# Kernel optimization log

Measured on AMD Instinct MI355X. Metric: run time of the kernel, lower is better.

## Reference

```python
import jax, jax.numpy as jnp
import numpy as np

B, D_IN, H1, H2, A = 8192, 512, 4096, 4096, 64
QMIN, QMAX = -128.0, 127.0  # int8 saturation range


def _int_vals(key, shape, spread):
    # integer-valued fixed-point tensor stored as float32
    return jnp.clip(jnp.round(jax.random.normal(key, shape) * spread), QMIN * spread, QMAX * spread).astype(jnp.float32)


def setup_inputs() -> dict:
    key = jax.random.key(0)
    ks = jax.random.split(key, 9)
    x = jnp.clip(jnp.round(jax.random.normal(ks[0], (B, D_IN)) * 32.0), QMIN, QMAX).astype(jnp.float32)
    w1 = jnp.clip(jnp.round(jax.random.normal(ks[1], (H1, D_IN)) * 16.0), QMIN, QMAX).astype(jnp.float32)
    b1 = _int_vals(ks[2], (H1,), 256.0)
    w2 = jnp.clip(jnp.round(jax.random.normal(ks[3], (H2, H1)) * 16.0), QMIN, QMAX).astype(jnp.float32)
    b2 = _int_vals(ks[4], (H2,), 256.0)
    w_mu = jnp.clip(jnp.round(jax.random.normal(ks[5], (A, H2)) * 16.0), QMIN, QMAX).astype(jnp.float32)
    b_mu = _int_vals(ks[6], (A,), 256.0)
    w_prob = jnp.clip(jnp.round(jax.random.normal(ks[7], (A, H2)) * 16.0), QMIN, QMAX).astype(jnp.float32)
    b_prob = _int_vals(ks[8], (A,), 256.0)
    M = jnp.full((1,), 2.0 ** -10, dtype=jnp.float32)  # per-layer requant multiplier
    s = jnp.full((1,), 0.05, dtype=jnp.float32)        # activation quantize scale
    return {
        "x": x, "w1": w1, "b1": b1, "w2": w2, "b2": b2,
        "w_mu": w_mu, "b_mu": b_mu, "w_prob": w_prob, "b_prob": b_prob,
        "M1": M, "M2": M, "M_mu": M, "M_prob": M,
        "s2": s, "s_mu": s, "s_prob": s,
    }


def _qlinear(x, w, b, M):
    # genesys fixed-point linear: int accumulate then requantize by multiplier M
    acc = jnp.matmul(x, w.T) + b  # integer-valued fp32 accumulator
    return jnp.round(M * acc)


def _quantize(src, scale, zero_point=0.0):
    return jnp.clip(jnp.round(src / scale) + zero_point, QMIN, QMAX)


def reference(x, w1, b1, w2, b2, w_mu, b_mu, w_prob, b_prob, M1, M2, M_mu, M_prob, s2, s_mu, s_prob):
    h = jax.nn.relu(_qlinear(x, w1, b1, M1))
    h = _quantize(h, s2)
    h = jax.nn.relu(_qlinear(h, w2, b2, M2))
    # NOTE: original forward_int feeds the un-quantized relu output into the
    # heads (x_mu/x_prob quantizations are dead code) and returns only prob.
    prob = _qlinear(h, w_prob, b_prob, M_prob)
    return prob
```

## Files before the change

kernel.cpp:

```cpp
#include <hip/hip_runtime.h>
#include <stdint.h>

#define NB   8192
#define DIN  512
#define NH1  4096
#define NH2  4096
#define NA   64

typedef int v4i __attribute__((ext_vector_type(4)));

__device__ __forceinline__ v4i mfma_i8(v4i a, v4i b, v4i c) {
    return __builtin_amdgcn_mfma_i32_16x16x64_i8(a, b, c, 0, 0, 0);
}

__device__ __forceinline__ void gload16(const void* g, const void* l) {
    __builtin_amdgcn_global_load_lds(
        (const __attribute__((address_space(1))) void*)(uintptr_t)g,
        (__attribute__((address_space(3))) void*)(uint32_t)(uintptr_t)l,
        16, 0, 0);
}

__global__ void cvt_i8(const float* __restrict__ in, signed char* __restrict__ out, int n4) {
    const int i = blockIdx.x * blockDim.x + threadIdx.x;
    if (i >= n4) return;
    const float4 v = ((const float4*)in)[i];
    char4 c;
    c.x = (signed char)__float2int_rn(v.x);
    c.y = (signed char)__float2int_rn(v.y);
    c.z = (signed char)__float2int_rn(v.z);
    c.w = (signed char)__float2int_rn(v.w);
    ((char4*)out)[i] = c;
}

__global__ void sum_wp(const float* __restrict__ wp, int* __restrict__ S) {
    __shared__ int red[256];
    const int a = blockIdx.x, t = threadIdx.x;
    int p = 0;
    for (int k = t; k < NH2; k += 256) p += __float2int_rn(wp[(size_t)a * NH2 + k]);
    red[t] = p; __syncthreads();
    for (int s = 128; s > 0; s >>= 1) { if (t < s) red[t] += red[t + s]; __syncthreads(); }
    if (t == 0) S[a] = red[0];
}

template <int EPI>
__global__ __launch_bounds__(512, 4)
void gemm_ra(const signed char* __restrict__ Ag,
             const signed char* __restrict__ Bg,
             int M, int N, int K,
             const float* __restrict__ bias,
             const float* __restrict__ Mscale,
             const float* __restrict__ qscale,
             signed char* __restrict__ out0,
             signed char* __restrict__ out1)
{
    __shared__ __align__(16) signed char lds[3][24576];

    const int tid  = threadIdx.x;
    const int lane = tid & 63;
    const int wid  = tid >> 6;
    const int wm   = wid >> 1, wn = wid & 1;

    const int nwg  = gridDim.x;
    const int bid  = blockIdx.x;
    const int swzb = (bid & 7) * (nwg >> 3) + (bid >> 3);
    const int nbx  = N >> 7;
    const int bx   = swzb % nbx;
    const int by   = swzb / nbx;
    const int bm0  = by << 8, bn0 = bx << 7;

    const int srow = tid >> 2;
    const int sc   = (((tid & 3) ^ ((tid >> 3) & 3)) << 4);
    const signed char* aS = Ag + (size_t)(bm0 + srow) * K + sc;
    const signed char* bS = Bg + (size_t)(bn0 + srow) * K + sc;
    const size_t rK = (size_t)128 * K;

#define STG(bp, t) do { \
    const int ko_ = (t) << 6; \
    gload16(aS + ko_,      &lds[bp][0]     + tid * 16); \
    gload16(aS + rK + ko_, &lds[bp][8192]  + tid * 16); \
    gload16(bS + ko_,      &lds[bp][16384] + tid * 16); } while (0)

    const int r    = lane & 15;
    const int pc   = (((lane >> 4) ^ ((r >> 1) & 3)) << 4);
    const int aoff = wm * 4096 + r * 64 + pc;
    const int boff = 16384 + wn * 4096 + r * 64 + pc;

    const int nt = K >> 6;

    STG(0, 0);
    STG(1, 1);
    asm volatile("s_waitcnt vmcnt(3)" ::: "memory");
    __builtin_amdgcn_s_barrier();

    v4i af[4], bf[4];
    {
        const signed char* L = &lds[0][0];
        #pragma unroll
        for (int m = 0; m < 4; ++m) af[m] = *(const v4i*)(L + aoff + m * 1024);
        #pragma unroll
        for (int n = 0; n < 4; ++n) bf[n] = *(const v4i*)(L + boff + n * 1024);
    }

    v4i acc[4][4] = {};
    int cur = 0;

    for (int t = 0; t < nt; ++t) {
        if (t + 2 < nt) {
            const int nb = (cur == 0) ? 2 : cur - 1;
            STG(nb, t + 2);
            asm volatile("s_waitcnt vmcnt(3)" ::: "memory");
        } else {
            asm volatile("s_waitcnt vmcnt(0)" ::: "memory");
        }
        __builtin_amdgcn_s_barrier();

        const int nxt = (cur == 2) ? 0 : cur + 1;
        const signed char* Ln = &lds[nxt][0];

        __builtin_amdgcn_s_setprio(1);
        #pragma unroll
        for (int m = 0; m < 4; ++m) {
            #pragma unroll
            for (int n = 0; n < 4; ++n)
                acc[m][n] = mfma_i8(af[m], bf[n], acc[m][n]);
            af[m] = *(const v4i*)(Ln + aoff + m * 1024);
        }
        __builtin_amdgcn_s_setprio(0);
        #pragma unroll
        for (int n = 0; n < 4; ++n) bf[n] = *(const v4i*)(Ln + boff + n * 1024);

        cur = nxt;
    }
#undef STG

    __syncthreads();
    signed char* img0 = (signed char*)&lds[0][0];
    signed char* img1 = img0 + 34816;
    const int rowb = wm * 64 + ((lane >> 4) << 2);
    const int colb = wn * 64 + (lane & 15);

#define FLUSH(dst, img) do { \
    _Pragma("unroll") \
    for (int p = 0; p < 8; ++p) { \
        const int idx = p * 512 + tid; \
        const int row = idx >> 4; \
        const int cb  = (idx & 15) * 8; \
        *(int2*)((dst) + (size_t)(bm0 + row) * N + bn0 + cb) = \
            *(const int2*)((img) + row * 136 + cb); \
    } } while (0)

    if constexpr (EPI == 1) {
        const float Mv = Mscale[0];
        const float sv = qscale[0];
        #pragma unroll
        for (int n = 0; n < 4; ++n) {
            const int col  = colb + n * 16;
            const int bint = __float2int_rn(bias[bn0 + col]);
            #pragma unroll
            for (int m = 0; m < 4; ++m) {
                #pragma unroll
                for (int j = 0; j < 4; ++j) {
                    const int row  = rowb + m * 16 + j;
                    const int accv = acc[m][n][j] + bint;
                    float h = rintf(Mv * (float)accv);
                    h = fmaxf(h, 0.0f);
                    float q = rintf(h / sv);
                    q = fminf(fmaxf(q, -128.0f), 127.0f);
                    img0[row * 136 + col] = (signed char)(int)q;
                }
            }
        }
        __syncthreads();
        FLUSH(out0, img0);
    } else {
        const float Mv = Mscale[0];
        #pragma unroll
        for (int n = 0; n < 4; ++n) {
            const int col  = colb + n * 16;
            const int bint = __float2int_rn(bias[bn0 + col]);
            #pragma unroll
            for (int m = 0; m < 4; ++m) {
                #pragma unroll
                for (int j = 0; j < 4; ++j) {
                    const int row  = rowb + m * 16 + j;
                    const int accv = acc[m][n][j] + bint;
                    double rr = rint((double)Mv * (double)accv);
                    rr = rr > 0.0 ? rr : 0.0;
                    const int v = (int)rr;
                    img0[row * 136 + col] = (signed char)((v & 255) - 128);
                    img1[row * 136 + col] = (signed char)((v >> 8) - 128);
                }
            }
        }
        __syncthreads();
        FLUSH(out0, img0);
        FLUSH(out1, img1);
    }
#undef FLUSH
}

__global__ __launch_bounds__(512, 1)
void head_mfma(const signed char* __restrict__ lo,
               const signed char* __restrict__ hi,
               const signed char* __restrict__ wpq,
               int* __restrict__ part)
{
    __shared__ __align__(16) signed char Bl[32768];
    __shared__ __align__(16) signed char Al[3][32768];

    const int tid  = threadIdx.x;
    const int lane = tid & 63;
    const int wid  = tid >> 6;
    const int rblk = blockIdx.x >> 3;
    const int kblk = blockIdx.x & 7;
    const int bm0  = rblk << 8;
    const int kb   = kblk << 9;

    #pragma unroll
    for (int s = 0; s < 4; ++s) {
        const int brow = s * 16 + (tid >> 5);
        const int pch  = tid & 31;
        const int lc   = pch ^ (brow & 7);
        gload16(wpq + (size_t)brow * NH2 + kb + lc * 16, Bl + brow * 512 + pch * 16);
    }

    const int srow  = tid >> 2;
    const int sclog = (tid & 3) ^ ((tid >> 3) & 3);
    const size_t ab = (size_t)(bm0 + srow) * NH2 + kb + sclog * 16;
    const size_t rK = (size_t)128 * NH2;

    #define HSTAGE(bp, ko) do { \
        gload16(lo + ab + (ko),      &Al[bp][0]     + tid * 16); \
        gload16(lo + ab + rK + (ko), &Al[bp][8192]  + tid * 16); \
        gload16(hi + ab + (ko),      &Al[bp][16384] + tid * 16); \
        gload16(hi + ab + rK + (ko), &Al[bp][24576] + tid * 16); } while (0)

    HSTAGE(0, 0);
    HSTAGE(1, 64);

    const int r    = lane & 15;
    const int cg   = lane >> 4;
    const int pcA  = (cg ^ ((r >> 1) & 3)) * 16;
    const int aoff = wid * 2048 + r * 64 + pcA;

    v4i accL[2][4] = {}, accH[2][4] = {};
    int cur = 0, nxt = 2;

    for (int t = 0; t < 8; ++t) {
        if (t < 7) asm volatile("s_waitcnt vmcnt(4)" ::: "memory");
        else       asm volatile("s_waitcnt vmcnt(0)" ::: "memory");
        __builtin_amdgcn_s_barrier();

        const signed char* A = &Al[cur][0];
        v4i bf[4], al[2], ah[2];
        #pragma unroll
        for (int n = 0; n < 4; ++n)
            bf[n] = *(const v4i*)(Bl + (n * 16 + r) * 512 + (((t * 4 + cg) ^ (r & 7)) * 16));
        #pragma unroll
        for (int m = 0; m < 2; ++m) al[m] = *(const v4i*)(A + aoff + m * 1024);
        #pragma unroll
        for (int m = 0; m < 2; ++m) ah[m] = *(const v4i*)(A + 16384 + aoff + m * 1024);

        if (t + 2 < 8) HSTAGE(nxt, (t + 2) << 6);

        __builtin_amdgcn_s_setprio(1);
        #pragma unroll
        for (int m = 0; m < 2; ++m)
            #pragma unroll
            for (int n = 0; n < 4; ++n) {
                accL[m][n] = mfma_i8(al[m], bf[n], accL[m][n]);
                accH[m][n] = mfma_i8(ah[m], bf[n], accH[m][n]);
            }
        __builtin_amdgcn_s_setprio(0);
        __builtin_amdgcn_s_barrier();

        cur = (cur == 2) ? 0 : cur + 1;
        nxt = (nxt == 2) ? 0 : nxt + 1;
    }
    #undef HSTAGE

    int* pb = part + (size_t)kblk * (NB * NA);
    const int rowb = bm0 + wid * 32 + ((lane >> 4) << 2);
    #pragma unroll
    for (int m = 0; m < 2; ++m)
        #pragma unroll
        for (int n = 0; n < 4; ++n) {
            const int a = n * 16 + (lane & 15);
            #pragma unroll
            for (int j = 0; j < 4; ++j) {
                const int row = rowb + m * 16 + j;
                pb[(size_t)row * NA + a] = accL[m][n][j] + (accH[m][n][j] << 8);
            }
        }
}

__global__ __launch_bounds__(256)
void comb_head(const int* __restrict__ part, const int* __restrict__ S,
               const float* __restrict__ bp, const float* __restrict__ Mp,
               float* __restrict__ out)
{
    const int t = blockIdx.x * 256 + threadIdx.x;
    const int a = t & 63;
    long long sum = 0;
    #pragma unroll
    for (int c = 0; c < 8; ++c) sum += part[(size_t)c * (NB * NA) + t];
    sum += 32896LL * (long long)S[a] + (long long)__float2int_rn(bp[a]);
    out[t] = (float)rint((double)Mp[0] * (double)sum);
}

extern "C" void kernel_launch(void* const* d_in, const int* in_sizes, int n_in,
                              void* d_out, int out_size, void* d_ws, size_t ws_size,
                              hipStream_t stream) {
    const float* x  = (const float*)d_in[0];
    const float* w1 = (const float*)d_in[1];
    const float* b1 = (const float*)d_in[2];
    const float* w2 = (const float*)d_in[3];
    const float* b2 = (const float*)d_in[4];
    const float* wp = (const float*)d_in[7];
    const float* bp = (const float*)d_in[8];
    const float* M1 = (const float*)d_in[9];
    const float* M2 = (const float*)d_in[10];
    const float* Mp = (const float*)d_in[12];
    const float* s2 = (const float*)d_in[13];

    const size_t MB = (size_t)1 << 20;
    char* ws = (char*)d_ws;
    signed char* x_i8  = (signed char*)(ws);
    signed char* w1_i8 = (signed char*)(ws + 4  * MB);
    signed char* w2_i8 = (signed char*)(ws + 6  * MB);
    signed char* wp_i8 = (signed char*)(ws + 22 * MB);
    int*         Ssum  = (int*)        (ws + 22 * MB + 512 * 1024);
    signed char* h1q   = (signed char*)(ws + 23 * MB);
    signed char* h2lo  = (signed char*)(ws + 55 * MB);
    signed char* h2hi  = (signed char*)(ws + 87 * MB);
    int*         part  = (int*)        (ws);

    cvt_i8<<<dim3(4096),  dim3(256), 0, stream>>>(x,  x_i8,  NB  * DIN / 4);
    cvt_i8<<<dim3(2048),  dim3(256), 0, stream>>>(w1, w1_i8, NH1 * DIN / 4);
    cvt_i8<<<dim3(16384), dim3(256), 0, stream>>>(w2, w2_i8, NH2 * NH1 / 4);
    cvt_i8<<<dim3(256),   dim3(256), 0, stream>>>(wp, wp_i8, NA  * NH2 / 4);
    sum_wp<<<dim3(64), dim3(256), 0, stream>>>(wp, Ssum);

    gemm_ra<1><<<dim3((NB / 256) * (NH1 / 128)), dim3(512), 0, stream>>>(
        x_i8, w1_i8, NB, NH1, DIN, b1, M1, s2, h1q, nullptr);
    gemm_ra<2><<<dim3((NB / 256) * (NH2 / 128)), dim3(512), 0, stream>>>(
        h1q, w2_i8, NB, NH2, NH1, b2, M2, nullptr, h2lo, h2hi);
    head_mfma<<<dim3(256), dim3(512), 0, stream>>>(h2lo, h2hi, wp_i8, part);
    comb_head<<<dim3(NB * NA / 256), dim3(256), 0, stream>>>(part, Ssum, bp, Mp, (float*)d_out);
}
```

Baseline: 230.1 us.

## Store activations in MFMA fragment layout and load A operand directly from global

The A operand (input x and first hidden layer) is now written in a pre-swizzled per-lane MFMA fragment layout, so each wave loads its A fragments straight from global memory into registers instead of staging them through LDS. Only the B (weight) tile is still staged in a three-buffer LDS pipeline, which shrinks LDS traffic and per-stage barrier data. The first GEMM epilogue writes its output directly in the fragment layout so the second GEMM consumes it the same way. The cost is that every wave of a block fetches its A rows from global/L2, with no sharing through LDS, and exposed global load latency on the A path.

After: 208.8 us. 1.1x faster.

```diff
diff --git a/kernel.cpp b/kernel.cpp
--- a/kernel.cpp
+++ b/kernel.cpp
@@ -32,6 +32,27 @@
     ((char4*)out)[i] = c;
 }
 
+__global__ void cvt_xfrag(const float* __restrict__ x, signed char* __restrict__ xf) {
+    const int u   = blockIdx.x * 256 + threadIdx.x;
+    const int g   = u >> 9;
+    const int rem = u & 511;
+    const int kt  = rem >> 6;
+    const int l   = rem & 63;
+    const int row = g * 16 + (l & 15);
+    const int k0  = kt * 64 + (l >> 4) * 16;
+    const float4* src = (const float4*)(x + (size_t)row * DIN + k0);
+    signed char v[16];
+    #pragma unroll
+    for (int q = 0; q < 4; ++q) {
+        const float4 f = src[q];
+        v[q*4+0] = (signed char)__float2int_rn(f.x);
+        v[q*4+1] = (signed char)__float2int_rn(f.y);
+        v[q*4+2] = (signed char)__float2int_rn(f.z);
+        v[q*4+3] = (signed char)__float2int_rn(f.w);
+    }
+    *(int4*)(xf + (size_t)u * 16) = *(const int4*)v;
+}
+
 __global__ void sum_wp(const float* __restrict__ wp, int* __restrict__ S) {
     __shared__ int red[256];
     const int a = blockIdx.x, t = threadIdx.x;
@@ -44,7 +65,7 @@
 
 template <int EPI>
 __global__ __launch_bounds__(512, 4)
-void gemm_ra(const signed char* __restrict__ Ag,
+void gemm_af(const signed char* __restrict__ Af,
              const signed char* __restrict__ Bg,
              int M, int N, int K,
              const float* __restrict__ bias,
@@ -53,7 +74,7 @@
              signed char* __restrict__ out0,
              signed char* __restrict__ out1)
 {
-    __shared__ __align__(16) signed char lds[3][24576];
+    __shared__ __align__(16) signed char lds[69632];
 
     const int tid  = threadIdx.x;
     const int lane = tid & 63;
@@ -70,52 +91,34 @@
 
     const int srow = tid >> 2;
     const int sc   = (((tid & 3) ^ ((tid >> 3) & 3)) << 4);
-    const signed char* aS = Ag + (size_t)(bm0 + srow) * K + sc;
     const signed char* bS = Bg + (size_t)(bn0 + srow) * K + sc;
-    const size_t rK = (size_t)128 * K;
-
-#define STG(bp, t) do { \
-    const int ko_ = (t) << 6; \
-    gload16(aS + ko_,      &lds[bp][0]     + tid * 16); \
-    gload16(aS + rK + ko_, &lds[bp][8192]  + tid * 16); \
-    gload16(bS + ko_,      &lds[bp][16384] + tid * 16); } while (0)
 
     const int r    = lane & 15;
     const int pc   = (((lane >> 4) ^ ((r >> 1) & 3)) << 4);
-    const int aoff = wm * 4096 + r * 64 + pc;
-    const int boff = 16384 + wn * 4096 + r * 64 + pc;
+    const int boff = wn * 4096 + r * 64 + pc;
+
+    const int NKT = K >> 6;
+    const signed char* afB = Af + (((size_t)((bm0 >> 4) + wm * 4) * NKT) << 10) + lane * 16;
 
     const int nt = K >> 6;
 
-    STG(0, 0);
-    STG(1, 1);
-    asm volatile("s_waitcnt vmcnt(3)" ::: "memory");
+    v4i af[4], bf[4];
+    #pragma unroll
+    for (int m = 0; m < 4; ++m)
+        af[m] = *(const v4i*)(afB + (((size_t)(m * NKT)) << 10));
+    gload16(bS,      lds + tid * 16);
+    gload16(bS + 64, lds + 8192 + tid * 16);
+    asm volatile("s_waitcnt vmcnt(1)" ::: "memory");
     __builtin_amdgcn_s_barrier();
 
-    v4i af[4], bf[4];
-    {
-        const signed char* L = &lds[0][0];
-        #pragma unroll
-        for (int m = 0; m < 4; ++m) af[m] = *(const v4i*)(L + aoff + m * 1024);
+    v4i acc[4][4] = {};
+
+    for (int t = 0; t < nt; ++t) {
+        const signed char* L = lds + (t % 3) * 8192;
         #pragma unroll
         for (int n = 0; n < 4; ++n) bf[n] = *(const v4i*)(L + boff + n * 1024);
-    }
-
-    v4i acc[4][4] = {};
-    int cur = 0;
-
-    for (int t = 0; t < nt; ++t) {
-        if (t + 2 < nt) {
-            const int nb = (cur == 0) ? 2 : cur - 1;
-            STG(nb, t + 2);
-            asm volatile("s_waitcnt vmcnt(3)" ::: "memory");
-        } else {
-            asm volatile("s_waitcnt vmcnt(0)" ::: "memory");
-        }
-        __builtin_amdgcn_s_barrier();
-
-        const int nxt = (cur == 2) ? 0 : cur + 1;
-        const signed char* Ln = &lds[nxt][0];
+
+        const size_t tl = (size_t)((t + 1 < nt) ? (t + 1) : t);
 
         __builtin_amdgcn_s_setprio(1);
         #pragma unroll
@@ -123,31 +126,24 @@
             #pragma unroll
             for (int n = 0; n < 4; ++n)
                 acc[m][n] = mfma_i8(af[m], bf[n], acc[m][n]);
-            af[m] = *(const v4i*)(Ln + aoff + m * 1024);
+            af[m] = *(const v4i*)(afB + (((size_t)(m * NKT) + tl) << 10));
         }
         __builtin_amdgcn_s_setprio(0);
-        #pragma unroll
-        for (int n = 0; n < 4; ++n) bf[n] = *(const v4i*)(Ln + boff + n * 1024);
-
-        cur = nxt;
-    }
-#undef STG
+
+        if (t + 2 < nt) {
+            gload16(bS + ((t + 2) << 6), lds + ((t + 2) % 3) * 8192 + tid * 16);
+            asm volatile("s_waitcnt vmcnt(1)" ::: "memory");
+        } else if (t + 1 < nt) {
+            asm volatile("s_waitcnt vmcnt(0)" ::: "memory");
+        }
+        __builtin_amdgcn_s_barrier();
+    }
 
     __syncthreads();
-    signed char* img0 = (signed char*)&lds[0][0];
-    signed char* img1 = img0 + 34816;
+    signed char* img0 = lds;
+    signed char* img1 = lds + 34816;
     const int rowb = wm * 64 + ((lane >> 4) << 2);
     const int colb = wn * 64 + (lane & 15);
-
-#define FLUSH(dst, img) do { \
-    _Pragma("unroll") \
-    for (int p = 0; p < 8; ++p) { \
-        const int idx = p * 512 + tid; \
-        const int row = idx >> 4; \
-        const int cb  = (idx & 15) * 8; \
-        *(int2*)((dst) + (size_t)(bm0 + row) * N + bn0 + cb) = \
-            *(const int2*)((img) + row * 136 + cb); \
-    } } while (0)
 
     if constexpr (EPI == 1) {
         const float Mv = Mscale[0];
@@ -171,7 +167,20 @@
             }
         }
         __syncthreads();
-        FLUSH(out0, img0);
+        const int oNKT = N >> 6;
+        #pragma unroll
+        for (int i = 0; i < 4; ++i) {
+            const int u    = i * 512 + tid;
+            const int g_l  = u >> 7;
+            const int kt_l = (u >> 6) & 1;
+            const int l    = u & 63;
+            const int lrow = g_l * 16 + (l & 15);
+            const int lcol = kt_l * 64 + (l >> 4) * 16;
+            const size_t g  = (size_t)((bm0 >> 4) + g_l);
+            const size_t kt = (size_t)((bn0 >> 6) + kt_l);
+            *(int4*)(out0 + ((g * oNKT + kt) << 10) + l * 16) =
+                *(const int4*)(img0 + lrow * 136 + lcol);
+        }
     } else {
         const float Mv = Mscale[0];
         #pragma unroll
@@ -193,10 +202,16 @@
             }
         }
         __syncthreads();
-        FLUSH(out0, img0);
-        FLUSH(out1, img1);
-    }
-#undef FLUSH
+        #pragma unroll
+        for (int p = 0; p < 8; ++p) {
+            const int idx = p * 512 + tid;
+            const int row = idx >> 4;
+            const int cb  = (idx & 15) * 8;
+            const size_t gaddr = (size_t)(bm0 + row) * N + bn0 + cb;
+            *(int2*)(out0 + gaddr) = *(const int2*)(img0 + row * 136 + cb);
+            *(int2*)(out1 + gaddr) = *(const int2*)(img1 + row * 136 + cb);
+        }
+    }
 }
 
 __global__ __launch_bounds__(512, 1)
@@ -325,26 +340,26 @@
 
     const size_t MB = (size_t)1 << 20;
     char* ws = (char*)d_ws;
-    signed char* x_i8  = (signed char*)(ws);
+    signed char* xf    = (signed char*)(ws);
     signed char* w1_i8 = (signed char*)(ws + 4  * MB);
     signed char* w2_i8 = (signed char*)(ws + 6  * MB);
     signed char* wp_i8 = (signed char*)(ws + 22 * MB);
     int*         Ssum  = (int*)        (ws + 22 * MB + 512 * 1024);
-    signed char* h1q   = (signed char*)(ws + 23 * MB);
+    signed char* h1f   = (signed char*)(ws + 23 * MB);
     signed char* h2lo  = (signed char*)(ws + 55 * MB);
     signed char* h2hi  = (signed char*)(ws + 87 * MB);
     int*         part  = (int*)        (ws);
 
-    cvt_i8<<<dim3(4096),  dim3(256), 0, stream>>>(x,  x_i8,  NB  * DIN / 4);
+    cvt_xfrag<<<dim3(1024), dim3(256), 0, stream>>>(x, xf);
     cvt_i8<<<dim3(2048),  dim3(256), 0, stream>>>(w1, w1_i8, NH1 * DIN / 4);
     cvt_i8<<<dim3(16384), dim3(256), 0, stream>>>(w2, w2_i8, NH2 * NH1 / 4);
     cvt_i8<<<dim3(256),   dim3(256), 0, stream>>>(wp, wp_i8, NA  * NH2 / 4);
     sum_wp<<<dim3(64), dim3(256), 0, stream>>>(wp, Ssum);
 
-    gemm_ra<1><<<dim3((NB / 256) * (NH1 / 128)), dim3(512), 0, stream>>>(
-        x_i8, w1_i8, NB, NH1, DIN, b1, M1, s2, h1q, nullptr);
-    gemm_ra<2><<<dim3((NB / 256) * (NH2 / 128)), dim3(512), 0, stream>>>(
-        h1q, w2_i8, NB, NH2, NH1, b2, M2, nullptr, h2lo, h2hi);
+    gemm_af<1><<<dim3((NB / 256) * (NH1 / 128)), dim3(512), 0, stream>>>(
+        xf, w1_i8, NB, NH1, DIN, b1, M1, s2, h1f, nullptr);
+    gemm_af<2><<<dim3((NB / 256) * (NH2 / 128)), dim3(512), 0, stream>>>(
+        h1f, w2_i8, NB, NH2, NH1, b2, M2, nullptr, h2lo, h2hi);
     head_mfma<<<dim3(256), dim3(512), 0, stream>>>(h2lo, h2hi, wp_i8, part);
     comb_head<<<dim3(NB * NA / 256), dim3(256), 0, stream>>>(part, Ssum, bp, Mp, (float*)d_out);
 }
```
